# Kernel tuning notes

Measured on AMD Instinct MI355X. Metric: run time of the kernel, lower is better.

Reference implementation:

```python
import jax, jax.numpy as jnp
import numpy as np

N, E, IN, H, L, NB, G = 50000, 300000, 64, 256, 4, 181, 64
EPS = 1e-5
NEG_SLOPE = 0.2


def segment_softmax(e, seg, n):
    m = jax.ops.segment_max(e, seg, num_segments=n)
    a = jnp.exp(e - m[seg])
    d = jax.ops.segment_sum(a, seg, num_segments=n)
    return a / d[seg]


def setup_inputs() -> dict:
    key = jax.random.key(0)
    ks = jax.random.split(key, 32)
    p = lambda k, shape, fan: (jax.random.normal(k, shape, jnp.float32) / np.sqrt(fan)).astype(jnp.float32)
    inp = {}
    inp["x"] = jax.random.normal(ks[0], (N, IN), jnp.float32)
    inp["edge_index"] = jax.random.randint(ks[1], (2, E), 0, N, jnp.int64)
    inp["batch"] = jnp.sort(jax.random.randint(ks[2], (N,), 0, G, jnp.int64))
    inp["W_in"] = p(ks[3], (H, IN), IN); inp["b_in"] = jnp.zeros((H,), jnp.float32)
    inp["Wl"] = p(ks[4], (L, H, H), H); inp["bl"] = jnp.zeros((L, H), jnp.float32)
    inp["Wr"] = p(ks[5], (L, H, H), H); inp["br"] = jnp.zeros((L, H), jnp.float32)
    inp["att"] = p(ks[6], (L, H), H)
    inp["bias_c"] = jnp.zeros((L, H), jnp.float32)
    inp["ln_g"] = jnp.ones((L, H), jnp.float32); inp["ln_b"] = jnp.zeros((L, H), jnp.float32)
    inp["Wg1"] = p(ks[7], (H, H), H); inp["bg1"] = jnp.zeros((H,), jnp.float32)
    inp["Wg2"] = p(ks[8], (1, H), H); inp["bg2"] = jnp.zeros((1,), jnp.float32)
    inp["Ws"] = p(ks[9], (H, H), H); inp["bs"] = jnp.zeros((H,), jnp.float32)
    inp["Wc"] = p(ks[10], (NB, H), H); inp["bc"] = jnp.zeros((NB,), jnp.float32)
    inp["Wr1"] = p(ks[11], (128, H), H); inp["br1"] = jnp.zeros((128,), jnp.float32)
    inp["Wr2"] = p(ks[12], (1, 128), 128); inp["br2"] = jnp.zeros((1,), jnp.float32)
    return inp


def reference(x, edge_index, batch, W_in, b_in, Wl, bl, Wr, br, att, bias_c, ln_g, ln_b,
              Wg1, bg1, Wg2, bg2, Ws, bs, Wc, bc, Wr1, br1, Wr2, br2):
    n = x.shape[0]
    x = x @ W_in.T + b_in  # input projection -> [N,H]
    loops = jnp.arange(n)
    src = jnp.concatenate([edge_index[0], loops])  # GATv2 add_self_loops=True
    dst = jnp.concatenate([edge_index[1], loops])
    for l in range(L):
        x_res = x
        xl = x @ Wl[l].T + bl[l]  # lin_l (source)
        xr = x @ Wr[l].T + br[l]  # lin_r (target)
        h = jax.nn.leaky_relu(xl[src] + xr[dst], NEG_SLOPE)  # [E+N, H]
        e = h @ att[l]                                       # [E+N]
        alpha = segment_softmax(e, dst, n)
        out = jax.ops.segment_sum(alpha[:, None] * xl[src], dst, num_segments=n) + bias_c[l]
        mu = out.mean(-1, keepdims=True)
        var = out.var(-1, keepdims=True)
        out = (out - mu) / jnp.sqrt(var + EPS) * ln_g[l] + ln_b[l]
        x = jax.nn.relu(out) + x_res  # dropout is identity at eval
    gate = jax.nn.relu(x @ Wg1.T + bg1) @ Wg2.T + bg2  # [N,1]
    a = segment_softmax(gate[:, 0], batch, G)
    pooled = jax.ops.segment_sum(a[:, None] * x, batch, num_segments=G)  # [G,H]
    z = jax.nn.relu(pooled @ Ws.T + bs)
    cls_logits = z @ Wc.T + bc                                   # [G,NB]
    residual = jnp.tanh(jax.nn.relu(z @ Wr1.T + br1) @ Wr2.T + br2)[:, 0]  # [G]
    return cls_logits, residual
```

## Files before the change

### kernel.cpp

```cpp
#include <hip/hip_runtime.h>
#include <math.h>

#define N_NODES 50000
#define N_EDGES 300000
#define IN_DIM 64
#define H 256
#define LAYERS 4
#define NB 181
#define NGRAPH 64
#define EE (N_EDGES + N_NODES)
#define NEG_SLOPE 0.2f
#define LN_EPS 1e-5f

typedef unsigned short u16;
typedef __attribute__((ext_vector_type(8))) _Float16 half8;
typedef __attribute__((ext_vector_type(4))) float floatx4;

__device__ __forceinline__ u16 f2h(float f) {
  _Float16 h = (_Float16)f;
  return __builtin_bit_cast(u16, h);
}
__device__ __forceinline__ float h2f(u16 b) {
  return (float)__builtin_bit_cast(_Float16, b);
}

__device__ __forceinline__ float wave_reduce_sum(float v) {
  #pragma unroll
  for (int off = 32; off > 0; off >>= 1) v += __shfl_xor(v, off, 64);
  return v;
}

__global__ void cast_weights_kernel(
    const float* __restrict__ Wg1,
    const float* __restrict__ Wl, const float* __restrict__ Wr,
    u16* __restrict__ wg1_h, u16* __restrict__ wl_h, u16* __restrict__ wr_h)
{
  int i = blockIdx.x * 256 + threadIdx.x;
  int which = blockIdx.y;
  const float* s; u16* dd; int n4;
  if (which == 0)      { s = Wg1;  dd = wg1_h; n4 = H * H / 4; }
  else if (which == 1) { s = Wl;   dd = wl_h;  n4 = LAYERS * H * H / 4; }
  else                 { s = Wr;   dd = wr_h;  n4 = LAYERS * H * H / 4; }
  if (i < n4) {
    float4 f = ((const float4*)s)[i];
    ushort4 o;
    o.x = f2h(f.x); o.y = f2h(f.y); o.z = f2h(f.z); o.w = f2h(f.w);
    ((ushort4*)dd)[i] = o;
  }
}

__global__ void init_kernel(int* __restrict__ cnt,
                            float* __restrict__ gate, const float* __restrict__ bg2,
                            const int* __restrict__ batch,
                            int* __restrict__ gstart, int* __restrict__ gend) {
  int i = blockIdx.x * 256 + threadIdx.x;
  if (i < N_NODES) {
    cnt[i] = 1;
    gate[i] = bg2[0];
    int b = batch[i];
    if (i == 0 || batch[i - 1] != b) gstart[b] = i;
    if (i == N_NODES - 1 || batch[i + 1] != b) gend[b] = i + 1;
  }
}

__global__ void count_edges_kernel(const int* __restrict__ dst, int* __restrict__ cnt) {
  int e = blockIdx.x * 256 + threadIdx.x;
  if (e < N_EDGES) atomicAdd(&cnt[dst[e]], 1);
}

__global__ void scan_blocks_kernel(const int* __restrict__ cnt, int* __restrict__ partial,
                                   int* __restrict__ bsums, int n) {
  __shared__ int buf[256];
  int tid = threadIdx.x;
  int i = blockIdx.x * 256 + tid;
  buf[tid] = (i < n) ? cnt[i] : 0;
  __syncthreads();
  #pragma unroll
  for (int off = 1; off < 256; off <<= 1) {
    int t = (tid >= off) ? buf[tid - off] : 0;
    __syncthreads();
    buf[tid] += t;
    __syncthreads();
  }
  if (i < n) partial[i] = buf[tid];
  if (tid == 255) bsums[blockIdx.x] = buf[255];
}

__global__ void scan_sums_kernel(int* __restrict__ bsums, int nblk) {
  __shared__ int buf[256];
  int tid = threadIdx.x;
  buf[tid] = (tid < nblk) ? bsums[tid] : 0;
  __syncthreads();
  #pragma unroll
  for (int off = 1; off < 256; off <<= 1) {
    int t = (tid >= off) ? buf[tid - off] : 0;
    __syncthreads();
    buf[tid] += t;
    __syncthreads();
  }
  if (tid < nblk) bsums[tid] = buf[tid];
}

__global__ void scan_write_kernel(const int* __restrict__ partial, const int* __restrict__ bsums,
                                  const int* __restrict__ cnt,
                                  int* __restrict__ rowp, int* __restrict__ col,
                                  int* __restrict__ fillpos, int n) {
  int i = blockIdx.x * 256 + threadIdx.x;
  if (i < n) {
    int b = blockIdx.x;
    int off = (b > 0) ? bsums[b - 1] : 0;
    int r1 = partial[i] + off;
// ... 209 lines not shown
    const float* __restrict__ bias, const float* __restrict__ Wg2,
    float* __restrict__ gate, int M)
{
  __shared__ u16 As[DTM * LDB];
  __shared__ u16 Bs[128 * LDB];
  int tid = threadIdx.x;
  int lane = tid & 63;
  int wave = tid >> 6;
  int wn = wave * 32;
  int n0 = blockIdx.x * 128;
  int bm = blockIdx.y * DTM;
  int mrow = lane & 15;
  int q8 = (lane >> 4) * 8;
  int ccol = lane & 15;
  int crow4 = (lane >> 4) * 4;
  int lr = tid >> 3;
  int lc = (tid & 7) * 8;

  floatx4 zero4 = {0.f, 0.f, 0.f, 0.f};
  floatx4 acc[4][2];
  #pragma unroll
  for (int i = 0; i < 4; i++) {
    acc[i][0] = zero4;
    acc[i][1] = zero4;
  }

  for (int k0 = 0; k0 < H; k0 += 64) {
    __syncthreads();
    #pragma unroll
    for (int p = 0; p < 2; p++) {
      int row = lr + p * 32;
      int gr = bm + row;
      uint4 av = {0, 0, 0, 0};
      if (gr < M) av = *(const uint4*)&A[(size_t)gr * H + k0 + lc];
      *(uint4*)&As[row * LDB + lc] = av;
    }
    #pragma unroll
    for (int p = 0; p < 4; p++) {
      int row = lr + p * 32;
      uint4 bv = *(const uint4*)&W[(size_t)(n0 + row) * H + k0 + lc];
      *(uint4*)&Bs[row * LDB + lc] = bv;
    }
    __syncthreads();
    #pragma unroll
    for (int h = 0; h < 2; h++) {
      half8 af[4], bf[2];
      #pragma unroll
      for (int i = 0; i < 4; i++)
        af[i] = *(const half8*)&As[(i * 16 + mrow) * LDB + h * 32 + q8];
      #pragma unroll
      for (int j = 0; j < 2; j++)
        bf[j] = *(const half8*)&Bs[(wn + j * 16 + mrow) * LDB + h * 32 + q8];
      #pragma unroll
      for (int i = 0; i < 4; i++)
        #pragma unroll
        for (int j = 0; j < 2; j++)
          acc[i][j] = __builtin_amdgcn_mfma_f32_16x16x32_f16(af[i], bf[j], acc[i][j], 0, 0, 0);
    }
  }

  float bv[2], wv[2];
  #pragma unroll
  for (int j = 0; j < 2; j++) {
    int c = n0 + wn + j * 16 + ccol;
    bv[j] = bias[c];
    wv[j] = Wg2[c];
  }
  #pragma unroll
  for (int i = 0; i < 4; i++) {
    #pragma unroll
    for (int r = 0; r < 4; r++) {
      float p = fmaxf(acc[i][0][r] + bv[0], 0.f) * wv[0]
              + fmaxf(acc[i][1][r] + bv[1], 0.f) * wv[1];
      p += __shfl_xor(p, 1, 64);
      p += __shfl_xor(p, 2, 64);
      p += __shfl_xor(p, 4, 64);
      p += __shfl_xor(p, 8, 64);
      int row = bm + i * 16 + crow4 + r;
      if ((lane & 15) == 0 && row < M) atomicAdd(&gate[row], p);
    }
  }
}

__global__ __launch_bounds__(256) void layer_fused_kernel(
    const u16* __restrict__ xl, const u16* __restrict__ xr,
    u16* __restrict__ xst,
    const int* __restrict__ rowp, const int* __restrict__ col,
    const float* __restrict__ att, const float* __restrict__ bias_c,
    const float* __restrict__ ln_g, const float* __restrict__ ln_b)
{
  int lane = threadIdx.x & 63;
  int v = blockIdx.x * 4 + (threadIdx.x >> 6);
  if (v >= N_NODES) return;
  int f4 = lane << 2;
  size_t rowbase = (size_t)v * H;
  ushort4 xr4 = *(const ushort4*)&xr[rowbase + f4];
  float xrx = h2f(xr4.x), xry = h2f(xr4.y), xrz = h2f(xr4.z), xrw = h2f(xr4.w);
  float4 attv = *(const float4*)&att[f4];
  int beg = rowp[v], end = rowp[v + 1];

  float sx, sy, sz, sw, m;
  {
    ushort4 a04 = *(const ushort4*)&xl[rowbase + f4];
    sx = h2f(a04.x); sy = h2f(a04.y); sz = h2f(a04.z); sw = h2f(a04.w);
    float t0x = sx + xrx; t0x = t0x > 0.f ? t0x : NEG_SLOPE * t0x;
    float t0y = sy + xry; t0y = t0y > 0.f ? t0y : NEG_SLOPE * t0y;
    float t0z = sz + xrz; t0z = t0z > 0.f ? t0z : NEG_SLOPE * t0z;
    float t0w = sw + xrw; t0w = t0w > 0.f ? t0w : NEG_SLOPE * t0w;
    float pe = t0x * attv.x + t0y * attv.y + t0z * attv.z + t0w * attv.w;
    m = wave_reduce_sum(pe);
  }
  float d = 1.0f;
  float ox = sx, oy = sy, oz = sz, ow = sw;

  int p = beg + 1;
  for (; p + 4 <= end; p += 4) {
    int u0 = col[p];
    int u1 = col[p + 1];
    int u2 = col[p + 2];
    int u3 = col[p + 3];
    ushort4 A0 = *(const ushort4*)&xl[(size_t)u0 * H + f4];
    ushort4 A1 = *(const ushort4*)&xl[(size_t)u1 * H + f4];
    ushort4 A2 = *(const ushort4*)&xl[(size_t)u2 * H + f4];
    ushort4 A3 = *(const ushort4*)&xl[(size_t)u3 * H + f4];
    float a0x = h2f(A0.x), a0y = h2f(A0.y), a0z = h2f(A0.z), a0w = h2f(A0.w);
    float a1x = h2f(A1.x), a1y = h2f(A1.y), a1z = h2f(A1.z), a1w = h2f(A1.w);
    float a2x = h2f(A2.x), a2y = h2f(A2.y), a2z = h2f(A2.z), a2w = h2f(A2.w);
    float a3x = h2f(A3.x), a3y = h2f(A3.y), a3z = h2f(A3.z), a3w = h2f(A3.w);
    float t, pe0, pe1, pe2, pe3;
    t = a0x + xrx; t = t > 0.f ? t : NEG_SLOPE * t; pe0 = t * attv.x;
    t = a0y + xry; t = t > 0.f ? t : NEG_SLOPE * t; pe0 = fmaf(t, attv.y, pe0);
    t = a0z + xrz; t = t > 0.f ? t : NEG_SLOPE * t; pe0 = fmaf(t, attv.z, pe0);
    t = a0w + xrw; t = t > 0.f ? t : NEG_SLOPE * t; pe0 = fmaf(t, attv.w, pe0);
    t = a1x + xrx; t = t > 0.f ? t : NEG_SLOPE * t; pe1 = t * attv.x;
    t = a1y + xry; t = t > 0.f ? t : NEG_SLOPE * t; pe1 = fmaf(t, attv.y, pe1);
    t = a1z + xrz; t = t > 0.f ? t : NEG_SLOPE * t; pe1 = fmaf(t, attv.z, pe1);
    t = a1w + xrw; t = t > 0.f ? t : NEG_SLOPE * t; pe1 = fmaf(t, attv.w, pe1);
    t = a2x + xrx; t = t > 0.f ? t : NEG_SLOPE * t; pe2 = t * attv.x;
    t = a2y + xry; t = t > 0.f ? t : NEG_SLOPE * t; pe2 = fmaf(t, attv.y, pe2);
    t = a2z + xrz; t = t > 0.f ? t : NEG_SLOPE * t; pe2 = fmaf(t, attv.z, pe2);
    t = a2w + xrw; t = t > 0.f ? t : NEG_SLOPE * t; pe2 = fmaf(t, attv.w, pe2);
    t = a3x + xrx; t = t > 0.f ? t : NEG_SLOPE * t; pe3 = t * attv.x;
    t = a3y + xry; t = t > 0.f ? t : NEG_SLOPE * t; pe3 = fmaf(t, attv.y, pe3);
    t = a3z + xrz; t = t > 0.f ? t : NEG_SLOPE * t; pe3 = fmaf(t, attv.z, pe3);
    t = a3w + xrw; t = t > 0.f ? t : NEG_SLOPE * t; pe3 = fmaf(t, attv.w, pe3);
    #pragma unroll
    for (int off = 32; off > 0; off >>= 1) {
      pe0 += __shfl_xor(pe0, off, 64);
      pe1 += __shfl_xor(pe1, off, 64);
      pe2 += __shfl_xor(pe2, off, 64);
      pe3 += __shfl_xor(pe3, off, 64);
    }
    float w0 = __expf(pe0 - m);
    float w1 = __expf(pe1 - m);
    float w2 = __expf(pe2 - m);
    float w3 = __expf(pe3 - m);
    d += (w0 + w1) + (w2 + w3);
    ox = fmaf(w0, a0x, fmaf(w1, a1x, fmaf(w2, a2x, fmaf(w3, a3x, ox))));
    oy = fmaf(w0, a0y, fmaf(w1, a1y, fmaf(w2, a2y, fmaf(w3, a3y, oy))));
    oz = fmaf(w0, a0z, fmaf(w1, a1z, fmaf(w2, a2z, fmaf(w3, a3z, oz))));
    ow = fmaf(w0, a0w, fmaf(w1, a1w, fmaf(w2, a2w, fmaf(w3, a3w, ow))));
  }
  for (; p < end; p++) {
    int u0 = col[p];
    ushort4 a04 = *(const ushort4*)&xl[(size_t)u0 * H + f4];
    float a0x = h2f(a04.x), a0y = h2f(a04.y), a0z = h2f(a04.z), a0w = h2f(a04.w);
    float t0x = a0x + xrx; t0x = t0x > 0.f ? t0x : NEG_SLOPE * t0x;
    float t0y = a0y + xry; t0y = t0y > 0.f ? t0y : NEG_SLOPE * t0y;
    float t0z = a0z + xrz; t0z = t0z > 0.f ? t0z : NEG_SLOPE * t0z;
    float t0w = a0w + xrw; t0w = t0w > 0.f ? t0w : NEG_SLOPE * t0w;
    float pe0 = t0x * attv.x + t0y * attv.y + t0z * attv.z + t0w * attv.w;
    pe0 = wave_reduce_sum(pe0);
    float w0 = __expf(pe0 - m);
    d += w0;
    ox = fmaf(w0, a0x, ox);
    oy = fmaf(w0, a0y, oy);
    oz = fmaf(w0, a0z, oz);
    ow = fmaf(w0, a0w, ow);
  }
  float invd = 1.0f / d;
  float4 bc4 = *(const float4*)&bias_c[f4];
  ox = ox * invd + bc4.x;
  oy = oy * invd + bc4.y;
  oz = oz * invd + bc4.z;
  ow = ow * invd + bc4.w;
  float s = wave_reduce_sum(ox + oy + oz + ow);
  float mean = s * (1.0f / H);
  float cx = ox - mean, cy = oy - mean, cz = oz - mean, cw = ow - mean;
  float sq = wave_reduce_sum(cx * cx + cy * cy + cz * cz + cw * cw);
  float rstd = rsqrtf(sq * (1.0f / H) + LN_EPS);
  float4 g4 = *(const float4*)&ln_g[f4];
  float4 b4 = *(const float4*)&ln_b[f4];
  ushort4 xres4 = *(const ushort4*)&xst[rowbase + f4];
  float yx = fmaxf(fmaf(cx * rstd, g4.x, b4.x), 0.f) + h2f(xres4.x);
  float yy = fmaxf(fmaf(cy * rstd, g4.y, b4.y), 0.f) + h2f(xres4.y);
  float yz = fmaxf(fmaf(cz * rstd, g4.z, b4.z), 0.f) + h2f(xres4.z);
  float yw = fmaxf(fmaf(cw * rstd, g4.w, b4.w), 0.f) + h2f(xres4.w);
  ushort4 yb;
  yb.x = f2h(yx); yb.y = f2h(yy); yb.z = f2h(yz); yb.w = f2h(yw);
  *(ushort4*)&xst[rowbase + f4] = yb;
}

__global__ __launch_bounds__(256) void pool_prep_kernel(
    const float* __restrict__ gate, const int* __restrict__ gstart,
    const int* __restrict__ gend, float* __restrict__ gmax, float* __restrict__ gdinv,
    float* __restrict__ pooled)
{
  __shared__ float red[256];
  int g = blockIdx.x, tid = threadIdx.x;
  pooled[(size_t)g * H + tid] = 0.f;
  int s = gstart[g], e = gend[g];
  float lm = -INFINITY;
  for (int i = s + tid; i < e; i += 256) lm = fmaxf(lm, gate[i]);
  red[tid] = lm;
  __syncthreads();
  for (int off = 128; off; off >>= 1) {
    if (tid < off) red[tid] = fmaxf(red[tid], red[tid + off]);
    __syncthreads();
  }
  float m = red[0];
  __syncthreads();
  float lsum = 0.0f;
  for (int i = s + tid; i < e; i += 256) lsum += __expf(gate[i] - m);
  red[tid] = lsum;
  __syncthreads();
  for (int off = 128; off; off >>= 1) {
    if (tid < off) red[tid] += red[tid + off];
    __syncthreads();
  }
  if (tid == 0) {
    gmax[g] = m;
    gdinv[g] = (s < e) ? 1.0f / red[0] : 0.0f;
  }
}

__global__ __launch_bounds__(256) void pool_accum_kernel(
    const float* __restrict__ gate, const u16* __restrict__ xh,
    const int* __restrict__ batch, const float* __restrict__ gmax,
    const float* __restrict__ gdinv, float* __restrict__ pooled)
{
  __shared__ float wl[64];
  __shared__ int gl[64];
  int b0 = blockIdx.x * 64;
  int tid = threadIdx.x;
  if (tid < 64) {
    int v = b0 + tid;
    if (v < N_NODES) {
      int g = batch[v];
      gl[tid] = g;
      wl[tid] = __expf(gate[v] - gmax[g]) * gdinv[g];
    } else {
      gl[tid] = -1;
      wl[tid] = 0.f;
    }
  }
  __syncthreads();
  int cnt = min(64, N_NODES - b0);
  float acc = 0.f;
  int cur = gl[0];
  for (int j = 0; j < cnt; j++) {
    int g = gl[j];
    if (g != cur) {
      atomicAdd(&pooled[(size_t)cur * H + tid], acc);
      acc = 0.f;
      cur = g;
    }
    acc += wl[j] * h2f(xh[(size_t)(b0 + j) * H + tid]);
  }
  if (cur >= 0) atomicAdd(&pooled[(size_t)cur * H + tid], acc);
}

__global__ __launch_bounds__(256) void head_kernel(
    const float* __restrict__ pooled,
    const float* __restrict__ Ws, const float* __restrict__ bs,
    const float* __restrict__ Wc, const float* __restrict__ bc,
    const float* __restrict__ Wr1, const float* __restrict__ br1,
    const float* __restrict__ Wr2, const float* __restrict__ br2,
    float* __restrict__ out)
{
  __shared__ float psh[256];
  __shared__ float zsh[256];
  __shared__ float r1sh[128];
  int g = blockIdx.x, tid = threadIdx.x;
// ... 31 lines not shown
    r1sh[tid] = fmaxf(acc, 0.f);
  }
  __syncthreads();
  if (tid < 64) {
    float s2 = r1sh[tid] * Wr2[tid] + r1sh[tid + 64] * Wr2[tid + 64];
    s2 = wave_reduce_sum(s2);
    if (tid == 0) out[(size_t)NGRAPH * NB + g] = tanhf(s2 + br2[0]);
  }
}

extern "C" void kernel_launch(void* const* d_in, const int* in_sizes, int n_in,
                              void* d_out, int out_size, void* d_ws, size_t ws_size,
                              hipStream_t stream) {
  const float* x_in   = (const float*)d_in[0];
  const int*   eidx   = (const int*)d_in[1];
  const int*   batch  = (const int*)d_in[2];
  const float* W_in   = (const float*)d_in[3];
  const float* b_in   = (const float*)d_in[4];
  const float* Wl     = (const float*)d_in[5];
  const float* bl     = (const float*)d_in[6];
  const float* Wr     = (const float*)d_in[7];
  const float* br     = (const float*)d_in[8];
  const float* att    = (const float*)d_in[9];
  const float* bias_c = (const float*)d_in[10];
  const float* ln_g   = (const float*)d_in[11];
  const float* ln_b   = (const float*)d_in[12];
  const float* Wg1    = (const float*)d_in[13];
  const float* bg1    = (const float*)d_in[14];
  const float* Wg2    = (const float*)d_in[15];
  const float* bg2    = (const float*)d_in[16];
  const float* Ws     = (const float*)d_in[17];
  const float* bs     = (const float*)d_in[18];
  const float* Wc     = (const float*)d_in[19];
  const float* bc     = (const float*)d_in[20];
  const float* Wr1    = (const float*)d_in[21];
  const float* br1    = (const float*)d_in[22];
  const float* Wr2    = (const float*)d_in[23];
  const float* br2    = (const float*)d_in[24];
  float* out = (float*)d_out;

  char* w = (char*)d_ws;
  u16* x_h    = (u16*)w;    w += sizeof(u16) * (size_t)N_NODES * H;
  u16* xl_h   = (u16*)w;    w += sizeof(u16) * (size_t)N_NODES * H;
  u16* xr_h   = (u16*)w;    w += sizeof(u16) * (size_t)N_NODES * H;
  u16* wl_h   = (u16*)w;    w += sizeof(u16) * (size_t)LAYERS * H * H;
  u16* wr_h   = (u16*)w;    w += sizeof(u16) * (size_t)LAYERS * H * H;
  u16* wg1_h  = (u16*)w;    w += sizeof(u16) * (size_t)H * H;
  float* pooled = (float*)w; w += sizeof(float) * NGRAPH * H;
  float* gate = (float*)w;  w += sizeof(float) * N_NODES;
  float* gmax = (float*)w;  w += sizeof(float) * NGRAPH;
  float* gdinv= (float*)w;  w += sizeof(float) * NGRAPH;
  int* cnt    = (int*)w;    w += sizeof(int) * N_NODES;
  int* rowp   = (int*)w;    w += sizeof(int) * (N_NODES + 1);
  int* col    = (int*)w;    w += sizeof(int) * EE;
  int* partial= (int*)w;    w += sizeof(int) * N_NODES;
  int* bsums  = (int*)w;    w += sizeof(int) * 256;
  int* gstart = (int*)w;    w += sizeof(int) * NGRAPH;
  int* gend   = (int*)w;    w += sizeof(int) * NGRAPH;
  (void)ws_size; (void)n_in; (void)in_sizes; (void)out_size;

  const int* src = eidx;
  const int* dst = eidx + N_EDGES;
  int nblkN = (N_NODES + 255) / 256;
  int nblkE = (N_EDGES + 255) / 256;
  int mtiles = (N_NODES + GTM - 1) / GTM;
  int mtiles2 = (N_NODES + DTM - 1) / DTM;

  init_kernel<<<nblkN, 256, 0, stream>>>(cnt, gate, bg2, batch, gstart, gend);
  count_edges_kernel<<<nblkE, 256, 0, stream>>>(dst, cnt);
  scan_blocks_kernel<<<nblkN, 256, 0, stream>>>(cnt, partial, bsums, N_NODES);
  scan_sums_kernel<<<1, 256, 0, stream>>>(bsums, nblkN);
  scan_write_kernel<<<nblkN, 256, 0, stream>>>(partial, bsums, cnt, rowp, col, cnt, N_NODES);
  fill_edges_kernel<<<nblkE, 256, 0, stream>>>(src, dst, cnt, col);

  {
    int maxn4 = LAYERS * H * H / 4;
    dim3 gcast((maxn4 + 255) / 256, 3);
    cast_weights_kernel<<<gcast, 256, 0, stream>>>(Wg1, Wl, Wr, wg1_h, wl_h, wr_h);
  }

  dim3 gproj(2, mtiles);
  gemm_proj_kernel<<<gproj, 256, 0, stream>>>(x_in, W_in, b_in, x_h, N_NODES);

  int nblkV = N_NODES / 4;
  dim3 gdual(4, mtiles2);
  for (int l = 0; l < LAYERS; l++) {
    gemm_dual3_kernel<<<gdual, 256, 0, stream>>>(x_h,
        wl_h + (size_t)l * H * H, wr_h + (size_t)l * H * H,
        bl + l * H, br + l * H, xl_h, xr_h, N_NODES);
    layer_fused_kernel<<<nblkV, 256, 0, stream>>>(xl_h, xr_h, x_h, rowp, col,
        att + l * H, bias_c + l * H, ln_g + l * H, ln_b + l * H);
  }

  dim3 ggate(2, mtiles2);
  gemm_gate2_kernel<<<ggate, 256, 0, stream>>>(x_h, wg1_h, bg1, Wg2, gate, N_NODES);

  pool_prep_kernel<<<NGRAPH, 256, 0, stream>>>(gate, gstart, gend, gmax, gdinv, pooled);
  pool_accum_kernel<<<(N_NODES + 63) / 64, 256, 0, stream>>>(gate, x_h, batch, gmax, gdinv, pooled);

  head_kernel<<<NGRAPH, 256, 0, stream>>>(pooled, Ws, bs, Wc, bc, Wr1, br1, Wr2, br2, out);
}
```

Measured before the change: 560.6 us.

## Use packed fp16 dot2 for GATv2 scores with grid-stride persistent node loop

Computes the leaky-relu attention logits in the per-node aggregation kernel with packed half2 add/max and the fdot2 instruction instead of scalar fp32 math, reducing ALU work per edge. The kernel launch becomes a fixed 2048-block grid-stride loop over nodes, so per-node constants (att, bias, LN params) are loaded once per wave. A 2-edge tail loop is also added. Doing the logit math in fp16 lowers precision of the attention scores, and the persistent grid may leave fewer waves in flight to hide gather latency.

```diff
diff --git a/kernel.cpp b/kernel.cpp
--- a/kernel.cpp
+++ b/kernel.cpp
@@ -15,6 +15,7 @@
 typedef unsigned short u16;
 typedef __attribute__((ext_vector_type(8))) _Float16 half8;
 typedef __attribute__((ext_vector_type(4))) float floatx4;
+typedef __attribute__((ext_vector_type(2))) _Float16 h2;
 
 __device__ __forceinline__ u16 f2h(float f) {
   _Float16 h = (_Float16)f;
@@ -22,6 +23,14 @@
 }
 __device__ __forceinline__ float h2f(u16 b) {
   return (float)__builtin_bit_cast(_Float16, b);
+}
+__device__ __forceinline__ h2 u2h2(unsigned int u) {
+  return __builtin_bit_cast(h2, u);
+}
+__device__ __forceinline__ float fdot2f(h2 a, h2 b, float c) {
+  typedef __attribute__((ext_vector_type(2))) __fp16 hb;
+  return __builtin_amdgcn_fdot2(__builtin_bit_cast(hb, a),
+                                __builtin_bit_cast(hb, b), c, false);
 }
 
 __device__ __forceinline__ float wave_reduce_sum(float v) {
@@ -402,6 +411,7 @@
   }
 }
 
+#define LF_BLOCKS 2048
 __global__ __launch_bounds__(256) void layer_fused_kernel(
     const u16* __restrict__ xl, const u16* __restrict__ xr,
     u16* __restrict__ xst,
@@ -410,115 +420,157 @@
     const float* __restrict__ ln_g, const float* __restrict__ ln_b)
 {
   int lane = threadIdx.x & 63;
-  int v = blockIdx.x * 4 + (threadIdx.x >> 6);
-  if (v >= N_NODES) return;
+  int wid = blockIdx.x * 4 + (threadIdx.x >> 6);
+  int nw = gridDim.x * 4;
   int f4 = lane << 2;
-  size_t rowbase = (size_t)v * H;
-  ushort4 xr4 = *(const ushort4*)&xr[rowbase + f4];
-  float xrx = h2f(xr4.x), xry = h2f(xr4.y), xrz = h2f(xr4.z), xrw = h2f(xr4.w);
+
   float4 attv = *(const float4*)&att[f4];
-  int beg = rowp[v], end = rowp[v + 1];
-
-  float sx, sy, sz, sw, m;
-  {
-    ushort4 a04 = *(const ushort4*)&xl[rowbase + f4];
-    sx = h2f(a04.x); sy = h2f(a04.y); sz = h2f(a04.z); sw = h2f(a04.w);
-    float t0x = sx + xrx; t0x = t0x > 0.f ? t0x : NEG_SLOPE * t0x;
-    float t0y = sy + xry; t0y = t0y > 0.f ? t0y : NEG_SLOPE * t0y;
-    float t0z = sz + xrz; t0z = t0z > 0.f ? t0z : NEG_SLOPE * t0z;
-    float t0w = sw + xrw; t0w = t0w > 0.f ? t0w : NEG_SLOPE * t0w;
-    float pe = t0x * attv.x + t0y * attv.y + t0z * attv.z + t0w * attv.w;
-    m = wave_reduce_sum(pe);
-  }
-  float d = 1.0f;
-  float ox = sx, oy = sy, oz = sz, ow = sw;
-
-  int p = beg + 1;
-  for (; p + 4 <= end; p += 4) {
-    int u0 = col[p];
-    int u1 = col[p + 1];
-    int u2 = col[p + 2];
-    int u3 = col[p + 3];
-    ushort4 A0 = *(const ushort4*)&xl[(size_t)u0 * H + f4];
-    ushort4 A1 = *(const ushort4*)&xl[(size_t)u1 * H + f4];
-    ushort4 A2 = *(const ushort4*)&xl[(size_t)u2 * H + f4];
-    ushort4 A3 = *(const ushort4*)&xl[(size_t)u3 * H + f4];
-    float a0x = h2f(A0.x), a0y = h2f(A0.y), a0z = h2f(A0.z), a0w = h2f(A0.w);
-    float a1x = h2f(A1.x), a1y = h2f(A1.y), a1z = h2f(A1.z), a1w = h2f(A1.w);
-    float a2x = h2f(A2.x), a2y = h2f(A2.y), a2z = h2f(A2.z), a2w = h2f(A2.w);
-    float a3x = h2f(A3.x), a3y = h2f(A3.y), a3z = h2f(A3.z), a3w = h2f(A3.w);
-    float t, pe0, pe1, pe2, pe3;
-    t = a0x + xrx; t = t > 0.f ? t : NEG_SLOPE * t; pe0 = t * attv.x;
-    t = a0y + xry; t = t > 0.f ? t : NEG_SLOPE * t; pe0 = fmaf(t, attv.y, pe0);
-    t = a0z + xrz; t = t > 0.f ? t : NEG_SLOPE * t; pe0 = fmaf(t, attv.z, pe0);
-    t = a0w + xrw; t = t > 0.f ? t : NEG_SLOPE * t; pe0 = fmaf(t, attv.w, pe0);
-    t = a1x + xrx; t = t > 0.f ? t : NEG_SLOPE * t; pe1 = t * attv.x;
-    t = a1y + xry; t = t > 0.f ? t : NEG_SLOPE * t; pe1 = fmaf(t, attv.y, pe1);
-    t = a1z + xrz; t = t > 0.f ? t : NEG_SLOPE * t; pe1 = fmaf(t, attv.z, pe1);
-    t = a1w + xrw; t = t > 0.f ? t : NEG_SLOPE * t; pe1 = fmaf(t, attv.w, pe1);
-    t = a2x + xrx; t = t > 0.f ? t : NEG_SLOPE * t; pe2 = t * attv.x;
-    t = a2y + xry; t = t > 0.f ? t : NEG_SLOPE * t; pe2 = fmaf(t, attv.y, pe2);
-    t = a2z + xrz; t = t > 0.f ? t : NEG_SLOPE * t; pe2 = fmaf(t, attv.z, pe2);
-    t = a2w + xrw; t = t > 0.f ? t : NEG_SLOPE * t; pe2 = fmaf(t, attv.w, pe2);
-    t = a3x + xrx; t = t > 0.f ? t : NEG_SLOPE * t; pe3 = t * attv.x;
-    t = a3y + xry; t = t > 0.f ? t : NEG_SLOPE * t; pe3 = fmaf(t, attv.y, pe3);
-    t = a3z + xrz; t = t > 0.f ? t : NEG_SLOPE * t; pe3 = fmaf(t, attv.z, pe3);
-    t = a3w + xrw; t = t > 0.f ? t : NEG_SLOPE * t; pe3 = fmaf(t, attv.w, pe3);
-    #pragma unroll
-    for (int off = 32; off > 0; off >>= 1) {
-      pe0 += __shfl_xor(pe0, off, 64);
-      pe1 += __shfl_xor(pe1, off, 64);
-      pe2 += __shfl_xor(pe2, off, 64);
-      pe3 += __shfl_xor(pe3, off, 64);
-    }
-    float w0 = __expf(pe0 - m);
-    float w1 = __expf(pe1 - m);
-    float w2 = __expf(pe2 - m);
-    float w3 = __expf(pe3 - m);
-    d += (w0 + w1) + (w2 + w3);
-    ox = fmaf(w0, a0x, fmaf(w1, a1x, fmaf(w2, a2x, fmaf(w3, a3x, ox))));
-    oy = fmaf(w0, a0y, fmaf(w1, a1y, fmaf(w2, a2y, fmaf(w3, a3y, oy))));
-    oz = fmaf(w0, a0z, fmaf(w1, a1z, fmaf(w2, a2z, fmaf(w3, a3z, oz))));
-    ow = fmaf(w0, a0w, fmaf(w1, a1w, fmaf(w2, a2w, fmaf(w3, a3w, ow))));
-  }
-  for (; p < end; p++) {
-    int u0 = col[p];
-    ushort4 a04 = *(const ushort4*)&xl[(size_t)u0 * H + f4];
-    float a0x = h2f(a04.x), a0y = h2f(a04.y), a0z = h2f(a04.z), a0w = h2f(a04.w);
-    float t0x = a0x + xrx; t0x = t0x > 0.f ? t0x : NEG_SLOPE * t0x;
-    float t0y = a0y + xry; t0y = t0y > 0.f ? t0y : NEG_SLOPE * t0y;
-    float t0z = a0z + xrz; t0z = t0z > 0.f ? t0z : NEG_SLOPE * t0z;
-    float t0w = a0w + xrw; t0w = t0w > 0.f ? t0w : NEG_SLOPE * t0w;
-    float pe0 = t0x * attv.x + t0y * attv.y + t0z * attv.z + t0w * attv.w;
-    pe0 = wave_reduce_sum(pe0);
-    float w0 = __expf(pe0 - m);
-    d += w0;
-    ox = fmaf(w0, a0x, ox);
-    oy = fmaf(w0, a0y, oy);
-    oz = fmaf(w0, a0z, oz);
-    ow = fmaf(w0, a0w, ow);
-  }
-  float invd = 1.0f / d;
+  h2 att01; att01[0] = (_Float16)attv.x; att01[1] = (_Float16)attv.y;
+  h2 att23; att23[0] = (_Float16)attv.z; att23[1] = (_Float16)attv.w;
+  h2 nsl;   nsl[0] = (_Float16)NEG_SLOPE; nsl[1] = (_Float16)NEG_SLOPE;
   float4 bc4 = *(const float4*)&bias_c[f4];
-  ox = ox * invd + bc4.x;
-  oy = oy * invd + bc4.y;
-  oz = oz * invd + bc4.z;
-  ow = ow * invd + bc4.w;
-  float s = wave_reduce_sum(ox + oy + oz + ow);
-  float mean = s * (1.0f / H);
-  float cx = ox - mean, cy = oy - mean, cz = oz - mean, cw = ow - mean;
-  float sq = wave_reduce_sum(cx * cx + cy * cy + cz * cz + cw * cw);
-  float rstd = rsqrtf(sq * (1.0f / H) + LN_EPS);
-  float4 g4 = *(const float4*)&ln_g[f4];
-  float4 b4 = *(const float4*)&ln_b[f4];
-  ushort4 xres4 = *(const ushort4*)&xst[rowbase + f4];
-  float yx = fmaxf(fmaf(cx * rstd, g4.x, b4.x), 0.f) + h2f(xres4.x);
-  float yy = fmaxf(fmaf(cy * rstd, g4.y, b4.y), 0.f) + h2f(xres4.y);
-  float yz = fmaxf(fmaf(cz * rstd, g4.z, b4.z), 0.f) + h2f(xres4.z);
-  float yw = fmaxf(fmaf(cw * rstd, g4.w, b4.w), 0.f) + h2f(xres4.w);
-  ushort4 yb;
-  yb.x = f2h(yx); yb.y = f2h(yy); yb.z = f2h(yz); yb.w = f2h(yw);
-  *(ushort4*)&xst[rowbase + f4] = yb;
+  float4 g4  = *(const float4*)&ln_g[f4];
+  float4 b4  = *(const float4*)&ln_b[f4];
+
+  for (int v = wid; v < N_NODES; v += nw) {
+    size_t rowbase = (size_t)v * H;
+    uint2 xru = *(const uint2*)&xr[rowbase + f4];
+    h2 xr01 = u2h2(xru.x), xr23 = u2h2(xru.y);
+    int beg = rowp[v], end = rowp[v + 1];
+
+    uint2 a0u = *(const uint2*)&xl[rowbase + f4];
+    h2 s01 = u2h2(a0u.x), s23 = u2h2(a0u.y);
+    float sx = (float)s01[0], sy = (float)s01[1];
+    float sz = (float)s23[0], sw = (float)s23[1];
+    float m;
+    {
+      h2 t0 = s01 + xr01;
+      h2 t1 = s23 + xr23;
+      h2 l0 = __builtin_elementwise_max(t0, t0 * nsl);
+      h2 l1 = __builtin_elementwise_max(t1, t1 * nsl);
+      float pe = fdot2f(l0, att01, 0.f);
+      pe = fdot2f(l1, att23, pe);
+      m = wave_reduce_sum(pe);
+    }
+    float d = 1.0f;
+    float ox = sx, oy = sy, oz = sz, ow = sw;
+
+    int p = beg + 1;
+    for (; p + 4 <= end; p += 4) {
+      int u0 = col[p];
+      int u1 = col[p + 1];
+      int u2 = col[p + 2];
+      int u3 = col[p + 3];
+      uint2 A0 = *(const uint2*)&xl[(size_t)u0 * H + f4];
+      uint2 A1 = *(const uint2*)&xl[(size_t)u1 * H + f4];
+      uint2 A2 = *(const uint2*)&xl[(size_t)u2 * H + f4];
+      uint2 A3 = *(const uint2*)&xl[(size_t)u3 * H + f4];
+      h2 a001 = u2h2(A0.x), a023 = u2h2(A0.y);
+      h2 a101 = u2h2(A1.x), a123 = u2h2(A1.y);
+      h2 a201 = u2h2(A2.x), a223 = u2h2(A2.y);
+      h2 a301 = u2h2(A3.x), a323 = u2h2(A3.y);
+      float pe0, pe1, pe2, pe3;
+      {
+        h2 t;
+        t = a001 + xr01; t = __builtin_elementwise_max(t, t * nsl); pe0 = fdot2f(t, att01, 0.f);
+        t = a023 + xr23; t = __builtin_elementwise_max(t, t * nsl); pe0 = fdot2f(t, att23, pe0);
+        t = a101 + xr01; t = __builtin_elementwise_max(t, t * nsl); pe1 = fdot2f(t, att01, 0.f);
+        t = a123 + xr23; t = __builtin_elementwise_max(t, t * nsl); pe1 = fdot2f(t, att23, pe1);
+        t = a201 + xr01; t = __builtin_elementwise_max(t, t * nsl); pe2 = fdot2f(t, att01, 0.f);
+        t = a223 + xr23; t = __builtin_elementwise_max(t, t * nsl); pe2 = fdot2f(t, att23, pe2);
+        t = a301 + xr01; t = __builtin_elementwise_max(t, t * nsl); pe3 = fdot2f(t, att01, 0.f);
+        t = a323 + xr23; t = __builtin_elementwise_max(t, t * nsl); pe3 = fdot2f(t, att23, pe3);
+      }
+      #pragma unroll
+      for (int off = 32; off > 0; off >>= 1) {
+        pe0 += __shfl_xor(pe0, off, 64);
+        pe1 += __shfl_xor(pe1, off, 64);
+        pe2 += __shfl_xor(pe2, off, 64);
+        pe3 += __shfl_xor(pe3, off, 64);
+      }
+      float w0 = __expf(pe0 - m);
+      float w1 = __expf(pe1 - m);
+      float w2 = __expf(pe2 - m);
+      float w3 = __expf(pe3 - m);
+      d += (w0 + w1) + (w2 + w3);
+      float a0x = (float)a001[0], a0y = (float)a001[1], a0z = (float)a023[0], a0w = (float)a023[1];
+      float a1x = (float)a101[0], a1y = (float)a101[1], a1z = (float)a123[0], a1w = (float)a123[1];
+      float a2x = (float)a201[0], a2y = (float)a201[1], a2z = (float)a223[0], a2w = (float)a223[1];
+      float a3x = (float)a301[0], a3y = (float)a301[1], a3z = (float)a323[0], a3w = (float)a323[1];
+      ox = fmaf(w0, a0x, fmaf(w1, a1x, fmaf(w2, a2x, fmaf(w3, a3x, ox))));
+      oy = fmaf(w0, a0y, fmaf(w1, a1y, fmaf(w2, a2y, fmaf(w3, a3y, oy))));
+      oz = fmaf(w0, a0z, fmaf(w1, a1z, fmaf(w2, a2z, fmaf(w3, a3z, oz))));
+      ow = fmaf(w0, a0w, fmaf(w1, a1w, fmaf(w2, a2w, fmaf(w3, a3w, ow))));
+    }
+    for (; p + 2 <= end; p += 2) {
+      int u0 = col[p];
+      int u1 = col[p + 1];
+      uint2 A0 = *(const uint2*)&xl[(size_t)u0 * H + f4];
+      uint2 A1 = *(const uint2*)&xl[(size_t)u1 * H + f4];
+      h2 a001 = u2h2(A0.x), a023 = u2h2(A0.y);
+      h2 a101 = u2h2(A1.x), a123 = u2h2(A1.y);
+      float pe0, pe1;
+      {
+        h2 t;
+        t = a001 + xr01; t = __builtin_elementwise_max(t, t * nsl); pe0 = fdot2f(t, att01, 0.f);
+        t = a023 + xr23; t = __builtin_elementwise_max(t, t * nsl); pe0 = fdot2f(t, att23, pe0);
+        t = a101 + xr01; t = __builtin_elementwise_max(t, t * nsl); pe1 = fdot2f(t, att01, 0.f);
+        t = a123 + xr23; t = __builtin_elementwise_max(t, t * nsl); pe1 = fdot2f(t, att23, pe1);
+      }
+      #pragma unroll
+      for (int off = 32; off > 0; off >>= 1) {
+        pe0 += __shfl_xor(pe0, off, 64);
+        pe1 += __shfl_xor(pe1, off, 64);
+      }
+      float w0 = __expf(pe0 - m);
+      float w1 = __expf(pe1 - m);
+      d += w0 + w1;
+      float a0x = (float)a001[0], a0y = (float)a001[1], a0z = (float)a023[0], a0w = (float)a023[1];
+      float a1x = (float)a101[0], a1y = (float)a101[1], a1z = (float)a123[0], a1w = (float)a123[1];
+      ox = fmaf(w0, a0x, fmaf(w1, a1x, ox));
+      oy = fmaf(w0, a0y, fmaf(w1, a1y, oy));
+      oz = fmaf(w0, a0z, fmaf(w1, a1z, oz));
+      ow = fmaf(w0, a0w, fmaf(w1, a1w, ow));
+    }
+    if (p < end) {
+      int u0 = col[p];
+      uint2 A0 = *(const uint2*)&xl[(size_t)u0 * H + f4];
+      h2 a001 = u2h2(A0.x), a023 = u2h2(A0.y);
+      float pe0;
+      {
+        h2 t;
+        t = a001 + xr01; t = __builtin_elementwise_max(t, t * nsl); pe0 = fdot2f(t, att01, 0.f);
+        t = a023 + xr23; t = __builtin_elementwise_max(t, t * nsl); pe0 = fdot2f(t, att23, pe0);
+      }
+      pe0 = wave_reduce_sum(pe0);
+      float w0 = __expf(pe0 - m);
+      d += w0;
+      float a0x = (float)a001[0], a0y = (float)a001[1], a0z = (float)a023[0], a0w = (float)a023[1];
+      ox = fmaf(w0, a0x, ox);
+      oy = fmaf(w0, a0y, oy);
+      oz = fmaf(w0, a0z, oz);
+      ow = fmaf(w0, a0w, ow);
+    }
+    float invd = 1.0f / d;
+    ox = ox * invd + bc4.x;
+    oy = oy * invd + bc4.y;
+    oz = oz * invd + bc4.z;
+    ow = ow * invd + bc4.w;
+    float s = wave_reduce_sum(ox + oy + oz + ow);
+    float mean = s * (1.0f / H);
+    float cx = ox - mean, cy = oy - mean, cz = oz - mean, cw = ow - mean;
+    float sq = wave_reduce_sum(cx * cx + cy * cy + cz * cz + cw * cw);
+    float rstd = rsqrtf(sq * (1.0f / H) + LN_EPS);
+    uint2 xres = *(const uint2*)&xst[rowbase + f4];
+    h2 r01 = u2h2(xres.x), r23 = u2h2(xres.y);
+    float yx = fmaxf(fmaf(cx * rstd, g4.x, b4.x), 0.f) + (float)r01[0];
+    float yy = fmaxf(fmaf(cy * rstd, g4.y, b4.y), 0.f) + (float)r01[1];
+    float yz = fmaxf(fmaf(cz * rstd, g4.z, b4.z), 0.f) + (float)r23[0];
+    float yw = fmaxf(fmaf(cw * rstd, g4.w, b4.w), 0.f) + (float)r23[1];
+    ushort4 yb;
+    yb.x = f2h(yx); yb.y = f2h(yy); yb.z = f2h(yz); yb.w = f2h(yw);
+    *(ushort4*)&xst[rowbase + f4] = yb;
+  }
 }
 
 __global__ __launch_bounds__(256) void pool_prep_kernel(
@@ -716,13 +768,12 @@
   dim3 gproj(2, mtiles);
   gemm_proj_kernel<<<gproj, 256, 0, stream>>>(x_in, W_in, b_in, x_h, N_NODES);
 
-  int nblkV = N_NODES / 4;
   dim3 gdual(4, mtiles2);
   for (int l = 0; l < LAYERS; l++) {
     gemm_dual3_kernel<<<gdual, 256, 0, stream>>>(x_h,
         wl_h + (size_t)l * H * H, wr_h + (size_t)l * H * H,
         bl + l * H, br + l * H, xl_h, xr_h, N_NODES);
-    layer_fused_kernel<<<nblkV, 256, 0, stream>>>(xl_h, xr_h, x_h, rowp, col,
+    layer_fused_kernel<<<LF_BLOCKS, 256, 0, stream>>>(xl_h, xr_h, x_h, rowp, col,
         att + l * H, bias_c + l * H, ln_g + l * H, ln_b + l * H);
   }
 
```

Result: slower. 595.9 us (+6.3%).

## Split GAT aggregation wave into two half-waves using packed fp16 dot2 math

Applied to the files above, without the earlier changes.

Each 64-lane wave now splits into two 32-lane halves. Each lane covers 8 features with 16-byte loads, and the two halves process different neighbor edges at the same time. The halves are merged with a cross-half shuffle before LayerNorm. Attention scores are computed with packed fp16 add/max and the fdot2 instruction, and the score reductions now need 5 shuffle steps instead of 6. This cuts per-edge shuffle and ALU cost and widens memory accesses. The trade-off is lower precision in the score computation and more work in the tail and merge paths.

```diff
diff --git a/kernel.cpp b/kernel.cpp
--- a/kernel.cpp
+++ b/kernel.cpp
@@ -15,6 +15,7 @@
 typedef unsigned short u16;
 typedef __attribute__((ext_vector_type(8))) _Float16 half8;
 typedef __attribute__((ext_vector_type(4))) float floatx4;
+typedef __attribute__((ext_vector_type(2))) _Float16 h2;
 
 __device__ __forceinline__ u16 f2h(float f) {
   _Float16 h = (_Float16)f;
@@ -23,10 +24,27 @@
 __device__ __forceinline__ float h2f(u16 b) {
   return (float)__builtin_bit_cast(_Float16, b);
 }
+__device__ __forceinline__ h2 u2h2(unsigned int u) {
+  return __builtin_bit_cast(h2, u);
+}
+__device__ __forceinline__ float fdot2f(h2 a, h2 b, float c) {
+  typedef __attribute__((ext_vector_type(2))) __fp16 hb;
+  return __builtin_amdgcn_fdot2(__builtin_bit_cast(hb, a),
+                                __builtin_bit_cast(hb, b), c, false);
+}
 
 __device__ __forceinline__ float wave_reduce_sum(float v) {
   #pragma unroll
   for (int off = 32; off > 0; off >>= 1) v += __shfl_xor(v, off, 64);
+  return v;
+}
+
+__device__ __forceinline__ float half_reduce_sum(float v) {
+  v += __shfl_xor(v, 1, 64);
+  v += __shfl_xor(v, 2, 64);
+  v += __shfl_xor(v, 4, 64);
+  v += __shfl_xor(v, 8, 64);
+  v += __shfl_xor(v, 16, 64);
   return v;
 }
 
@@ -412,113 +430,177 @@
   int lane = threadIdx.x & 63;
   int v = blockIdx.x * 4 + (threadIdx.x >> 6);
   if (v >= N_NODES) return;
-  int f4 = lane << 2;
-  size_t rowbase = (size_t)v * H;
-  ushort4 xr4 = *(const ushort4*)&xr[rowbase + f4];
-  float xrx = h2f(xr4.x), xry = h2f(xr4.y), xrz = h2f(xr4.z), xrw = h2f(xr4.w);
-  float4 attv = *(const float4*)&att[f4];
+  int half = lane >> 5;
+  int f8 = (lane & 31) << 3;
+
+  float4 attA = *(const float4*)&att[f8];
+  float4 attB = *(const float4*)&att[f8 + 4];
+  h2 att0, att1, att2, att3;
+  att0[0] = (_Float16)attA.x; att0[1] = (_Float16)attA.y;
+  att1[0] = (_Float16)attA.z; att1[1] = (_Float16)attA.w;
+  att2[0] = (_Float16)attB.x; att2[1] = (_Float16)attB.y;
+  att3[0] = (_Float16)attB.z; att3[1] = (_Float16)attB.w;
+  h2 nsl; nsl[0] = (_Float16)NEG_SLOPE; nsl[1] = (_Float16)NEG_SLOPE;
+
+  size_t rowbase = (size_t)v * H + f8;
+  uint4 xru = *(const uint4*)&xr[rowbase];
+  h2 xr0 = u2h2(xru.x), xr1 = u2h2(xru.y), xr2 = u2h2(xru.z), xr3 = u2h2(xru.w);
   int beg = rowp[v], end = rowp[v + 1];
 
-  float sx, sy, sz, sw, m;
+  uint4 su = *(const uint4*)&xl[rowbase];
+  h2 s0 = u2h2(su.x), s1 = u2h2(su.y), s2 = u2h2(su.z), s3 = u2h2(su.w);
+  float m;
   {
-    ushort4 a04 = *(const ushort4*)&xl[rowbase + f4];
-    sx = h2f(a04.x); sy = h2f(a04.y); sz = h2f(a04.z); sw = h2f(a04.w);
-    float t0x = sx + xrx; t0x = t0x > 0.f ? t0x : NEG_SLOPE * t0x;
-    float t0y = sy + xry; t0y = t0y > 0.f ? t0y : NEG_SLOPE * t0y;
-    float t0z = sz + xrz; t0z = t0z > 0.f ? t0z : NEG_SLOPE * t0z;
-    float t0w = sw + xrw; t0w = t0w > 0.f ? t0w : NEG_SLOPE * t0w;
-    float pe = t0x * attv.x + t0y * attv.y + t0z * attv.z + t0w * attv.w;
-    m = wave_reduce_sum(pe);
-  }
-  float d = 1.0f;
-  float ox = sx, oy = sy, oz = sz, ow = sw;
+    h2 t; float pe = 0.f;
+    t = s0 + xr0; t = __builtin_elementwise_max(t, t * nsl); pe = fdot2f(t, att0, pe);
+    t = s1 + xr1; t = __builtin_elementwise_max(t, t * nsl); pe = fdot2f(t, att1, pe);
+    t = s2 + xr2; t = __builtin_elementwise_max(t, t * nsl); pe = fdot2f(t, att2, pe);
+    t = s3 + xr3; t = __builtin_elementwise_max(t, t * nsl); pe = fdot2f(t, att3, pe);
+    m = half_reduce_sum(pe);
+  }
+  float wself = half ? 0.f : 1.f;
+  float d = wself;
+  float o0 = wself * (float)s0[0], o1 = wself * (float)s0[1];
+  float o2 = wself * (float)s1[0], o3 = wself * (float)s1[1];
+  float o4 = wself * (float)s2[0], o5 = wself * (float)s2[1];
+  float o6 = wself * (float)s3[0], o7 = wself * (float)s3[1];
 
   int p = beg + 1;
   for (; p + 4 <= end; p += 4) {
-    int u0 = col[p];
-    int u1 = col[p + 1];
-    int u2 = col[p + 2];
-    int u3 = col[p + 3];
-    ushort4 A0 = *(const ushort4*)&xl[(size_t)u0 * H + f4];
-    ushort4 A1 = *(const ushort4*)&xl[(size_t)u1 * H + f4];
-    ushort4 A2 = *(const ushort4*)&xl[(size_t)u2 * H + f4];
-    ushort4 A3 = *(const ushort4*)&xl[(size_t)u3 * H + f4];
-    float a0x = h2f(A0.x), a0y = h2f(A0.y), a0z = h2f(A0.z), a0w = h2f(A0.w);
-    float a1x = h2f(A1.x), a1y = h2f(A1.y), a1z = h2f(A1.z), a1w = h2f(A1.w);
-    float a2x = h2f(A2.x), a2y = h2f(A2.y), a2z = h2f(A2.z), a2w = h2f(A2.w);
-    float a3x = h2f(A3.x), a3y = h2f(A3.y), a3z = h2f(A3.z), a3w = h2f(A3.w);
-    float t, pe0, pe1, pe2, pe3;
-    t = a0x + xrx; t = t > 0.f ? t : NEG_SLOPE * t; pe0 = t * attv.x;
-    t = a0y + xry; t = t > 0.f ? t : NEG_SLOPE * t; pe0 = fmaf(t, attv.y, pe0);
-    t = a0z + xrz; t = t > 0.f ? t : NEG_SLOPE * t; pe0 = fmaf(t, attv.z, pe0);
-    t = a0w + xrw; t = t > 0.f ? t : NEG_SLOPE * t; pe0 = fmaf(t, attv.w, pe0);
-    t = a1x + xrx; t = t > 0.f ? t : NEG_SLOPE * t; pe1 = t * attv.x;
-    t = a1y + xry; t = t > 0.f ? t : NEG_SLOPE * t; pe1 = fmaf(t, attv.y, pe1);
-    t = a1z + xrz; t = t > 0.f ? t : NEG_SLOPE * t; pe1 = fmaf(t, attv.z, pe1);
-    t = a1w + xrw; t = t > 0.f ? t : NEG_SLOPE * t; pe1 = fmaf(t, attv.w, pe1);
-    t = a2x + xrx; t = t > 0.f ? t : NEG_SLOPE * t; pe2 = t * attv.x;
-    t = a2y + xry; t = t > 0.f ? t : NEG_SLOPE * t; pe2 = fmaf(t, attv.y, pe2);
-    t = a2z + xrz; t = t > 0.f ? t : NEG_SLOPE * t; pe2 = fmaf(t, attv.z, pe2);
-    t = a2w + xrw; t = t > 0.f ? t : NEG_SLOPE * t; pe2 = fmaf(t, attv.w, pe2);
-    t = a3x + xrx; t = t > 0.f ? t : NEG_SLOPE * t; pe3 = t * attv.x;
-    t = a3y + xry; t = t > 0.f ? t : NEG_SLOPE * t; pe3 = fmaf(t, attv.y, pe3);
-    t = a3z + xrz; t = t > 0.f ? t : NEG_SLOPE * t; pe3 = fmaf(t, attv.z, pe3);
-    t = a3w + xrw; t = t > 0.f ? t : NEG_SLOPE * t; pe3 = fmaf(t, attv.w, pe3);
-    #pragma unroll
-    for (int off = 32; off > 0; off >>= 1) {
-      pe0 += __shfl_xor(pe0, off, 64);
-      pe1 += __shfl_xor(pe1, off, 64);
-      pe2 += __shfl_xor(pe2, off, 64);
-      pe3 += __shfl_xor(pe3, off, 64);
-    }
-    float w0 = __expf(pe0 - m);
-    float w1 = __expf(pe1 - m);
-    float w2 = __expf(pe2 - m);
-    float w3 = __expf(pe3 - m);
-    d += (w0 + w1) + (w2 + w3);
-    ox = fmaf(w0, a0x, fmaf(w1, a1x, fmaf(w2, a2x, fmaf(w3, a3x, ox))));
-    oy = fmaf(w0, a0y, fmaf(w1, a1y, fmaf(w2, a2y, fmaf(w3, a3y, oy))));
-    oz = fmaf(w0, a0z, fmaf(w1, a1z, fmaf(w2, a2z, fmaf(w3, a3z, oz))));
-    ow = fmaf(w0, a0w, fmaf(w1, a1w, fmaf(w2, a2w, fmaf(w3, a3w, ow))));
-  }
-  for (; p < end; p++) {
-    int u0 = col[p];
-    ushort4 a04 = *(const ushort4*)&xl[(size_t)u0 * H + f4];
-    float a0x = h2f(a04.x), a0y = h2f(a04.y), a0z = h2f(a04.z), a0w = h2f(a04.w);
-    float t0x = a0x + xrx; t0x = t0x > 0.f ? t0x : NEG_SLOPE * t0x;
-    float t0y = a0y + xry; t0y = t0y > 0.f ? t0y : NEG_SLOPE * t0y;
-    float t0z = a0z + xrz; t0z = t0z > 0.f ? t0z : NEG_SLOPE * t0z;
-    float t0w = a0w + xrw; t0w = t0w > 0.f ? t0w : NEG_SLOPE * t0w;
-    float pe0 = t0x * attv.x + t0y * attv.y + t0z * attv.z + t0w * attv.w;
-    pe0 = wave_reduce_sum(pe0);
-    float w0 = __expf(pe0 - m);
-    d += w0;
-    ox = fmaf(w0, a0x, ox);
-    oy = fmaf(w0, a0y, oy);
-    oz = fmaf(w0, a0z, oz);
-    ow = fmaf(w0, a0w, ow);
-  }
+    int ua = col[p + half];
+    int ub = col[p + 2 + half];
+    uint4 A = *(const uint4*)&xl[(size_t)ua * H + f8];
+    uint4 B = *(const uint4*)&xl[(size_t)ub * H + f8];
+    h2 a0 = u2h2(A.x), a1 = u2h2(A.y), a2 = u2h2(A.z), a3 = u2h2(A.w);
+    h2 b0 = u2h2(B.x), b1 = u2h2(B.y), b2 = u2h2(B.z), b3 = u2h2(B.w);
+    float pa = 0.f, pb = 0.f;
+    {
+      h2 t;
+      t = a0 + xr0; t = __builtin_elementwise_max(t, t * nsl); pa = fdot2f(t, att0, pa);
+      t = b0 + xr0; t = __builtin_elementwise_max(t, t * nsl); pb = fdot2f(t, att0, pb);
+      t = a1 + xr1; t = __builtin_elementwise_max(t, t * nsl); pa = fdot2f(t, att1, pa);
+      t = b1 + xr1; t = __builtin_elementwise_max(t, t * nsl); pb = fdot2f(t, att1, pb);
+      t = a2 + xr2; t = __builtin_elementwise_max(t, t * nsl); pa = fdot2f(t, att2, pa);
+      t = b2 + xr2; t = __builtin_elementwise_max(t, t * nsl); pb = fdot2f(t, att2, pb);
+      t = a3 + xr3; t = __builtin_elementwise_max(t, t * nsl); pa = fdot2f(t, att3, pa);
+      t = b3 + xr3; t = __builtin_elementwise_max(t, t * nsl); pb = fdot2f(t, att3, pb);
+    }
+    #pragma unroll
+    for (int off = 1; off <= 16; off <<= 1) {
+      pa += __shfl_xor(pa, off, 64);
+      pb += __shfl_xor(pb, off, 64);
+    }
+    float wa = __expf(pa - m);
+    float wb = __expf(pb - m);
+    d += wa + wb;
+    o0 = fmaf(wa, (float)a0[0], fmaf(wb, (float)b0[0], o0));
+    o1 = fmaf(wa, (float)a0[1], fmaf(wb, (float)b0[1], o1));
+    o2 = fmaf(wa, (float)a1[0], fmaf(wb, (float)b1[0], o2));
+    o3 = fmaf(wa, (float)a1[1], fmaf(wb, (float)b1[1], o3));
+    o4 = fmaf(wa, (float)a2[0], fmaf(wb, (float)b2[0], o4));
+    o5 = fmaf(wa, (float)a2[1], fmaf(wb, (float)b2[1], o5));
+    o6 = fmaf(wa, (float)a3[0], fmaf(wb, (float)b3[0], o6));
+    o7 = fmaf(wa, (float)a3[1], fmaf(wb, (float)b3[1], o7));
+  }
+  for (; p + 2 <= end; p += 2) {
+    int ua = col[p + half];
+    uint4 A = *(const uint4*)&xl[(size_t)ua * H + f8];
+    h2 a0 = u2h2(A.x), a1 = u2h2(A.y), a2 = u2h2(A.z), a3 = u2h2(A.w);
+    float pa = 0.f;
+    {
+      h2 t;
+      t = a0 + xr0; t = __builtin_elementwise_max(t, t * nsl); pa = fdot2f(t, att0, pa);
+      t = a1 + xr1; t = __builtin_elementwise_max(t, t * nsl); pa = fdot2f(t, att1, pa);
+      t = a2 + xr2; t = __builtin_elementwise_max(t, t * nsl); pa = fdot2f(t, att2, pa);
+      t = a3 + xr3; t = __builtin_elementwise_max(t, t * nsl); pa = fdot2f(t, att3, pa);
+    }
+    pa = half_reduce_sum(pa);
+    float wa = __expf(pa - m);
+    d += wa;
+    o0 = fmaf(wa, (float)a0[0], o0);
+    o1 = fmaf(wa, (float)a0[1], o1);
+    o2 = fmaf(wa, (float)a1[0], o2);
+    o3 = fmaf(wa, (float)a1[1], o3);
+    o4 = fmaf(wa, (float)a2[0], o4);
+    o5 = fmaf(wa, (float)a2[1], o5);
+    o6 = fmaf(wa, (float)a3[0], o6);
+    o7 = fmaf(wa, (float)a3[1], o7);
+  }
+  if (p < end) {
+    int ua = col[p];
+    uint4 A = *(const uint4*)&xl[(size_t)ua * H + f8];
+    h2 a0 = u2h2(A.x), a1 = u2h2(A.y), a2 = u2h2(A.z), a3 = u2h2(A.w);
+    float pa = 0.f;
+    {
+      h2 t;
+      t = a0 + xr0; t = __builtin_elementwise_max(t, t * nsl); pa = fdot2f(t, att0, pa);
+      t = a1 + xr1; t = __builtin_elementwise_max(t, t * nsl); pa = fdot2f(t, att1, pa);
+      t = a2 + xr2; t = __builtin_elementwise_max(t, t * nsl); pa = fdot2f(t, att2, pa);
+      t = a3 + xr3; t = __builtin_elementwise_max(t, t * nsl); pa = fdot2f(t, att3, pa);
+    }
+    pa = half_reduce_sum(pa);
+    float wa = __expf(pa - m) * wself;
+    d += wa;
+    o0 = fmaf(wa, (float)a0[0], o0);
+    o1 = fmaf(wa, (float)a0[1], o1);
+    o2 = fmaf(wa, (float)a1[0], o2);
+    o3 = fmaf(wa, (float)a1[1], o3);
+    o4 = fmaf(wa, (float)a2[0], o4);
+    o5 = fmaf(wa, (float)a2[1], o5);
+    o6 = fmaf(wa, (float)a3[0], o6);
+    o7 = fmaf(wa, (float)a3[1], o7);
+  }
+
+  d += __shfl_xor(d, 32, 64);
+  o0 += __shfl_xor(o0, 32, 64);
+  o1 += __shfl_xor(o1, 32, 64);
+  o2 += __shfl_xor(o2, 32, 64);
+  o3 += __shfl_xor(o3, 32, 64);
+  o4 += __shfl_xor(o4, 32, 64);
+  o5 += __shfl_xor(o5, 32, 64);
+  o6 += __shfl_xor(o6, 32, 64);
+  o7 += __shfl_xor(o7, 32, 64);
+
   float invd = 1.0f / d;
-  float4 bc4 = *(const float4*)&bias_c[f4];
-  ox = ox * invd + bc4.x;
-  oy = oy * invd + bc4.y;
-  oz = oz * invd + bc4.z;
-  ow = ow * invd + bc4.w;
-  float s = wave_reduce_sum(ox + oy + oz + ow);
-  float mean = s * (1.0f / H);
-  float cx = ox - mean, cy = oy - mean, cz = oz - mean, cw = ow - mean;
-  float sq = wave_reduce_sum(cx * cx + cy * cy + cz * cz + cw * cw);
-  float rstd = rsqrtf(sq * (1.0f / H) + LN_EPS);
-  float4 g4 = *(const float4*)&ln_g[f4];
-  float4 b4 = *(const float4*)&ln_b[f4];
-  ushort4 xres4 = *(const ushort4*)&xst[rowbase + f4];
-  float yx = fmaxf(fmaf(cx * rstd, g4.x, b4.x), 0.f) + h2f(xres4.x);
-  float yy = fmaxf(fmaf(cy * rstd, g4.y, b4.y), 0.f) + h2f(xres4.y);
-  float yz = fmaxf(fmaf(cz * rstd, g4.z, b4.z), 0.f) + h2f(xres4.z);
-  float yw = fmaxf(fmaf(cw * rstd, g4.w, b4.w), 0.f) + h2f(xres4.w);
-  ushort4 yb;
-  yb.x = f2h(yx); yb.y = f2h(yy); yb.z = f2h(yz); yb.w = f2h(yw);
-  *(ushort4*)&xst[rowbase + f4] = yb;
+  float4 bcA = *(const float4*)&bias_c[f8];
+  float4 bcB = *(const float4*)&bias_c[f8 + 4];
+  o0 = o0 * invd + bcA.x; o1 = o1 * invd + bcA.y;
+  o2 = o2 * invd + bcA.z; o3 = o3 * invd + bcA.w;
+  o4 = o4 * invd + bcB.x; o5 = o5 * invd + bcB.y;
+  o6 = o6 * invd + bcB.z; o7 = o7 * invd + bcB.w;
+
+  float s = ((o0 + o1) + (o2 + o3)) + ((o4 + o5) + (o6 + o7));
+  s = wave_reduce_sum(s);
+  float mean = s * (1.0f / (2 * H));
+  float c0 = o0 - mean, c1 = o1 - mean, c2 = o2 - mean, c3 = o3 - mean;
+  float c4 = o4 - mean, c5 = o5 - mean, c6 = o6 - mean, c7 = o7 - mean;
+  float sq = ((c0 * c0 + c1 * c1) + (c2 * c2 + c3 * c3))
+           + ((c4 * c4 + c5 * c5) + (c6 * c6 + c7 * c7));
+  sq = wave_reduce_sum(sq);
+  float rstd = rsqrtf(sq * (1.0f / (2 * H)) + LN_EPS);
+
+  float4 gA = *(const float4*)&ln_g[f8];
+  float4 gB = *(const float4*)&ln_g[f8 + 4];
+  float4 bA = *(const float4*)&ln_b[f8];
+  float4 bB = *(const float4*)&ln_b[f8 + 4];
+  uint4 xres = *(const uint4*)&xst[rowbase];
+  h2 r0 = u2h2(xres.x), r1 = u2h2(xres.y), r2 = u2h2(xres.z), r3 = u2h2(xres.w);
+  float y0 = fmaxf(fmaf(c0 * rstd, gA.x, bA.x), 0.f) + (float)r0[0];
+  float y1 = fmaxf(fmaf(c1 * rstd, gA.y, bA.y), 0.f) + (float)r0[1];
+  float y2 = fmaxf(fmaf(c2 * rstd, gA.z, bA.z), 0.f) + (float)r1[0];
+  float y3 = fmaxf(fmaf(c3 * rstd, gA.w, bA.w), 0.f) + (float)r1[1];
+  float y4 = fmaxf(fmaf(c4 * rstd, gB.x, bB.x), 0.f) + (float)r2[0];
+  float y5 = fmaxf(fmaf(c5 * rstd, gB.y, bB.y), 0.f) + (float)r2[1];
+  float y6 = fmaxf(fmaf(c6 * rstd, gB.z, bB.z), 0.f) + (float)r3[0];
+  float y7 = fmaxf(fmaf(c7 * rstd, gB.w, bB.w), 0.f) + (float)r3[1];
+  if (!half) {
+    uint4 outv;
+    outv.x = (unsigned)f2h(y0) | ((unsigned)f2h(y1) << 16);
+    outv.y = (unsigned)f2h(y2) | ((unsigned)f2h(y3) << 16);
+    outv.z = (unsigned)f2h(y4) | ((unsigned)f2h(y5) << 16);
+    outv.w = (unsigned)f2h(y6) | ((unsigned)f2h(y7) << 16);
+    *(uint4*)&xst[rowbase] = outv;
+  }
 }
 
 __global__ __launch_bounds__(256) void pool_prep_kernel(
```

Result: no change. 559.7 us (-0.2%).
